# Optimization experiments

Hardware: AMD Instinct MI355X
Metric: run time of the kernel (lower is better)

Reference implementation:

```python
import jax, jax.numpy as jnp
import numpy as np

N_NODES = 50000
N_EDGES = 800000
F_IN = 128
HID = 128
OUT = 64


def setup_inputs() -> dict:
    key = jax.random.key(0)
    ks = jax.random.split(key, 10)
    def lin(k, fan_in, fan_out):
        s = 1.0 / np.sqrt(fan_in)
        kw, kb = jax.random.split(k)
        W = jax.random.uniform(kw, (fan_in, fan_out), jnp.float32, -s, s)
        b = jax.random.uniform(kb, (fan_out,), jnp.float32, -s, s)
        return W, b
    x = jax.random.normal(ks[0], (N_NODES, F_IN), jnp.float32)
    edge_index = jax.random.randint(ks[1], (2, N_EDGES), 0, N_NODES, dtype=jnp.int32)
    W1, b1 = lin(ks[2], F_IN, HID)   # GCNConv 1
    Wl, bl = lin(ks[3], HID, HID)    # linear_layers
    W2, b2 = lin(ks[4], HID, HID)    # GCNConv 2
    Wo, bo = lin(ks[5], HID, OUT)    # output_layers
    return {"x": x, "edge_index": edge_index, "W1": W1, "b1": b1,
            "Wl": Wl, "bl": bl, "W2": W2, "b2": b2, "Wo": Wo, "bo": bo}


def gcn_conv(x, src, dst, W, b, n_nodes):
    # PyG GCNConv: add self loops, symmetric norm D^-1/2 (A+I) D^-1/2 (x W) + b
    deg = jax.ops.segment_sum(jnp.ones_like(dst, dtype=x.dtype), dst, num_segments=n_nodes)
    dinv = jnp.where(deg > 0, jax.lax.rsqrt(jnp.maximum(deg, 1.0)), 0.0)
    norm = dinv[src] * dinv[dst]                     # [E+N]
    h = x @ W                                        # [N, H]
    msg = h[src] * norm[:, None]                     # [E+N, H]
    agg = jax.ops.segment_sum(msg, dst, num_segments=n_nodes)
    return agg + b


def reference(x, edge_index, W1, b1, Wl, bl, W2, b2, Wo, bo):
    n = x.shape[0]
    loops = jnp.arange(n, dtype=edge_index.dtype)
    src = jnp.concatenate([edge_index[0], loops])
    dst = jnp.concatenate([edge_index[1], loops])
    h = jnp.tanh(gcn_conv(x, src, dst, W1, b1, n))
    h = h @ Wl + bl
    h = jnp.tanh(gcn_conv(h, src, dst, W2, b2, n))
    h = h @ Wo + bo                                  # [N, OUT]
    # adaptive_max_pool1d over nodes -> [1, OUT]
    return jnp.max(h, axis=0, keepdims=True)
```

## Files before the change

### kernel.cpp

```cpp
#include <hip/hip_runtime.h>
#include <math.h>

#define F 128
#define OUTF 64
#define CAP 64

typedef __attribute__((ext_vector_type(8))) short short8;
typedef __attribute__((ext_vector_type(4))) float f32x4;

__device__ inline unsigned short bf16_rne(float f) {
    unsigned u = __float_as_uint(f);
    return (unsigned short)((u + 0x7FFFu + ((u >> 16) & 1u)) >> 16);
}
__device__ inline float bf16_to_f(unsigned short h) {
    return __uint_as_float((unsigned)h << 16);
}

__global__ __launch_bounds__(256)
void fill_kernel(const int* __restrict__ src, const int* __restrict__ dst,
                 int* __restrict__ cnt, int* __restrict__ slot, int E) {
    int e = blockIdx.x * 256 + threadIdx.x;
    if (e >= E) return;
    int s = src[e], d = dst[e];
    int pos = atomicAdd(&cnt[d], 1);
    if (pos < CAP) slot[(size_t)d * CAP + pos] = s;
}

__device__ inline void wsplit(float w, int k, int nn, short* Hh, short* Hl) {
    int c = k >> 5, hh = (k >> 3) & 3, kk = k & 7;
    int j = nn >> 4, col = nn & 15;
    int idx = (((j * 4 + c) * 4 + hh) * 16 + col) * 8 + kk;
    unsigned short hi = bf16_rne(w);
    Hh[idx] = (short)hi;
    Hl[idx] = (short)bf16_rne(w - bf16_to_f(hi));
}

__global__ __launch_bounds__(256)
void prep_kernel(const float* __restrict__ W1, const float* __restrict__ Wl,
                 const float* __restrict__ bl, const float* __restrict__ W2,
                 const float* __restrict__ Wo,
                 short* __restrict__ W1h, short* __restrict__ W1l,
                 short* __restrict__ Wfh, short* __restrict__ Wfl,
                 short* __restrict__ Woh, short* __restrict__ Wol,
                 float* __restrict__ bf, const int* __restrict__ cnt,
                 float* __restrict__ dinv, int n) {
    int bi = blockIdx.x, t = threadIdx.x;
    if (bi < 64) {
        int base = bi * 256 + t;
        int k = base >> 7, nn = base & 127;
        wsplit(W1[k * 128 + nn], k, nn, W1h, W1l);
    } else if (bi < 128) {
        int base = (bi - 64) * 256 + t;
        int k = base >> 7, nn = base & 127;
        float acc = 0.f;
        #pragma unroll 8
        for (int m = 0; m < 128; ++m)
            acc = fmaf(Wl[k * 128 + m], W2[m * 128 + nn], acc);
        wsplit(acc, k, nn, Wfh, Wfl);
    } else if (bi < 160) {
        int base = (bi - 128) * 256 + t;
        int k = base >> 6, nn = base & 63;
        wsplit(Wo[k * 64 + nn], k, nn, Woh, Wol);
    } else if (bi == 160) {
        if (t < 128) {
            float acc = 0.f;
            #pragma unroll 8
            for (int k = 0; k < 128; ++k)
                acc = fmaf(bl[k], W2[k * 128 + t], acc);
            bf[t] = acc;
        }
    } else {
        int i = (bi - 161) * 256 + t;
        if (i < n) dinv[i] = rsqrtf((float)cnt[i] + 1.0f);
    }
}

__global__ __launch_bounds__(256)
void gather_kernel(const float* __restrict__ H, const float* __restrict__ dinv,
                   const int* __restrict__ cnt, const int* __restrict__ slot,
                   const float* __restrict__ b, float* __restrict__ out, int n) {
    int wave = threadIdx.x >> 6;
    int lane = threadIdx.x & 63;
    int v = blockIdx.x * 4 + wave;
    if (v >= n) return;
    float dd = dinv[v];
    int deg = min(cnt[v], CAP);
    const int* sl = slot + (size_t)v * CAP;

    int s_l = 0; float nd_l = 0.f;
    if (lane < deg) { s_l = sl[lane]; nd_l = dinv[s_l] * dd; }

    float2 h0 = ((const float2*)(H + (size_t)v * F))[lane];
    float s2 = dd * dd;
    float ax = h0.x * s2, ay = h0.y * s2;

    int t = 0;
    for (; t + 4 <= deg; t += 4) {
        int s0 = __shfl(s_l, t),     s1 = __shfl(s_l, t + 1);
        int s2i = __shfl(s_l, t + 2), s3 = __shfl(s_l, t + 3);
        float n0 = __shfl(nd_l, t),     n1 = __shfl(nd_l, t + 1);
        float n2 = __shfl(nd_l, t + 2), n3 = __shfl(nd_l, t + 3);
        float2 u0 = ((const float2*)(H + (size_t)s0 * F))[lane];
        float2 u1 = ((const float2*)(H + (size_t)s1 * F))[lane];
        float2 u2 = ((const float2*)(H + (size_t)s2i * F))[lane];
        float2 u3 = ((const float2*)(H + (size_t)s3 * F))[lane];
        ax = fmaf(u0.x, n0, ax); ay = fmaf(u0.y, n0, ay);
        ax = fmaf(u1.x, n1, ax); ay = fmaf(u1.y, n1, ay);
        ax = fmaf(u2.x, n2, ax); ay = fmaf(u2.y, n2, ay);
        ax = fmaf(u3.x, n3, ax); ay = fmaf(u3.y, n3, ay);
    }
    for (; t < deg; ++t) {
        int s0 = __shfl(s_l, t);
        float n0 = __shfl(nd_l, t);
        float2 u0 = ((const float2*)(H + (size_t)s0 * F))[lane];
        ax = fmaf(u0.x, n0, ax); ay = fmaf(u0.y, n0, ay);
    }

    float2 bb = ((const float2*)b)[lane];
    float2 r;
    r.x = tanhf(ax + bb.x);
    r.y = tanhf(ay + bb.y);
    ((float2*)(out + (size_t)v * F))[lane] = r;
}

template<int COLS, bool BIAS, bool DOMAX>
__global__ __launch_bounds__(256)
void mgemm_kernel(const float* __restrict__ A, const short* __restrict__ Whi,
                  const short* __restrict__ Wlo, const float* __restrict__ bias,
                  float* __restrict__ C, float* __restrict__ part, int n) {
    constexpr int NT = COLS / 16;
    __shared__ float red[DOMAX ? 4 * COLS : 1];
    int t = threadIdx.x;
    int wave = t >> 6, l = t & 63;
    int fr = l & 15, fh = l >> 4;
    int m0 = blockIdx.x * 64 + wave * 16;
    int arow = min(m0 + fr, n - 1);
    const float* Ap = A + (size_t)arow * F + fh * 8;

    f32x4 acc[NT];
    #pragma unroll
    for (int j = 0; j < NT; ++j) acc[j] = (f32x4){0.f, 0.f, 0.f, 0.f};

    #pragma unroll
    for (int c = 0; c < 4; ++c) {
        float4 a0 = *(const float4*)(Ap + c * 32);
        float4 a1 = *(const float4*)(Ap + c * 32 + 4);
        short8 ahi, alo;
        {
            float v[8] = {a0.x, a0.y, a0.z, a0.w, a1.x, a1.y, a1.z, a1.w};
            #pragma unroll
            for (int i = 0; i < 8; ++i) {
                unsigned short hb = bf16_rne(v[i]);
                ahi[i] = (short)hb;
                alo[i] = (short)bf16_rne(v[i] - bf16_to_f(hb));
            }
        }
        #pragma unroll
        for (int j = 0; j < NT; ++j) {
            int bidx = (((j * 4 + c) * 4 + fh) * 16 + fr) * 8;
            short8 bhi = *(const short8*)(Whi + bidx);
            short8 blo = *(const short8*)(Wlo + bidx);
            acc[j] = __builtin_amdgcn_mfma_f32_16x16x32_bf16(ahi, bhi, acc[j], 0, 0, 0);
            acc[j] = __builtin_amdgcn_mfma_f32_16x16x32_bf16(alo, bhi, acc[j], 0, 0, 0);
            acc[j] = __builtin_amdgcn_mfma_f32_16x16x32_bf16(ahi, blo, acc[j], 0, 0, 0);
        }
    }

    float bv[NT];
    #pragma unroll
    for (int j = 0; j < NT; ++j) bv[j] = (BIAS || DOMAX) ? bias[j * 16 + fr] : 0.f;

    if (DOMAX) {
        #pragma unroll
        for (int j = 0; j < NT; ++j) {
            float mj = -INFINITY;
            #pragma unroll
            for (int reg = 0; reg < 4; ++reg) {
                int r = m0 + fh * 4 + reg;
                if (r < n) mj = fmaxf(mj, acc[j][reg] + bv[j]);
            }
            mj = fmaxf(mj, __shfl_xor(mj, 16));
            mj = fmaxf(mj, __shfl_xor(mj, 32));
            if (fh == 0) red[wave * COLS + j * 16 + fr] = mj;
        }
        __syncthreads();
        if (t < COLS) {
            float mm = fmaxf(fmaxf(red[t], red[COLS + t]),
                             fmaxf(red[2 * COLS + t], red[3 * COLS + t]));
            part[blockIdx.x * COLS + t] = mm;
        }
    } else {
        #pragma unroll
        for (int j = 0; j < NT; ++j) {
            int ccol = j * 16 + fr;
            #pragma unroll
            for (int reg = 0; reg < 4; ++reg) {
                int r = m0 + fh * 4 + reg;
                if (r < n) C[(size_t)r * COLS + ccol] = acc[j][reg] + bv[j];
            }
        }
    }
}

__global__ __launch_bounds__(256)
void rowmax_final(const float* __restrict__ part, float* __restrict__ out, int nb) {
    int c = threadIdx.x & 63;
    int g = threadIdx.x >> 6;
    float m = -INFINITY;
    for (int bidx = g; bidx < nb; bidx += 4)
        m = fmaxf(m, part[bidx * OUTF + c]);
    __shared__ float sm[256];
    sm[threadIdx.x] = m;
    __syncthreads();
    if (threadIdx.x < 64) {
        m = fmaxf(fmaxf(sm[threadIdx.x], sm[threadIdx.x + 64]),
                  fmaxf(sm[threadIdx.x + 128], sm[threadIdx.x + 192]));
        out[threadIdx.x] = m;
    }
}

extern "C" void kernel_launch(void* const* d_in, const int* in_sizes, int n_in,
                              void* d_out, int out_size, void* d_ws, size_t ws_size,
                              hipStream_t stream) {
    const float* x  = (const float*)d_in[0];
    const int*   ei = (const int*)d_in[1];
    const float* W1 = (const float*)d_in[2];
    const float* b1 = (const float*)d_in[3];
    const float* Wl = (const float*)d_in[4];
    const float* bl = (const float*)d_in[5];
    const float* W2 = (const float*)d_in[6];
    const float* b2 = (const float*)d_in[7];
    const float* Wo = (const float*)d_in[8];
    const float* bo = (const float*)d_in[9];

    int n = in_sizes[0] / F;
    int E = in_sizes[1] / 2;
    const int* src = ei;
    const int* dst = ei + E;

    auto align = [](size_t o) { return (o + 255) & ~(size_t)255; };
    char* ws = (char*)d_ws;
    size_t off = 0;
    size_t NB = (size_t)n * F * sizeof(float);
    float* bufA = (float*)(ws + off); off = align(off + NB);
    float* bufB = (float*)(ws + off); off = align(off + NB);
    float* dinv = (float*)(ws + off); off = align(off + (size_t)n * 4);
    int*   cnt  = (int*)(ws + off);   off = align(off + (size_t)n * 4);
    int*   slot = (int*)(ws + off);   off = align(off + (size_t)n * CAP * 4);
    float* bf   = (float*)(ws + off); off = align(off + 128 * 4);
    short* W1h  = (short*)(ws + off); off = align(off + 16384 * 2);
    short* W1l  = (short*)(ws + off); off = align(off + 16384 * 2);
    short* Wfh  = (short*)(ws + off); off = align(off + 16384 * 2);
    short* Wfl  = (short*)(ws + off); off = align(off + 16384 * 2);
    short* Woh  = (short*)(ws + off); off = align(off + 8192 * 2);
    short* Wol  = (short*)(ws + off); off = align(off + 8192 * 2);
    float* part = (float*)(ws + off); off = align(off + (size_t)800 * 64 * 4);

    int gE    = (E + 255) / 256;
    int gScan = (n + 255) / 256;
    int gGat  = (n + 3) / 4;
    int gM    = (n + 63) / 64;

    hipMemsetAsync(cnt, 0, (size_t)n * sizeof(int), stream);
    fill_kernel<<<gE, 256, 0, stream>>>(src, dst, cnt, slot, E);
    prep_kernel<<<161 + gScan, 256, 0, stream>>>(W1, Wl, bl, W2, Wo,
                                                 W1h, W1l, Wfh, Wfl, Woh, Wol,
                                                 bf, cnt, dinv, n);

    mgemm_kernel<128, false, false><<<gM, 256, 0, stream>>>(x, W1h, W1l, nullptr, bufA, nullptr, n);
    gather_kernel<<<gGat, 256, 0, stream>>>(bufA, dinv, cnt, slot, b1, bufB, n);

    mgemm_kernel<128, true, false><<<gM, 256, 0, stream>>>(bufB, Wfh, Wfl, bf, bufA, nullptr, n);
    gather_kernel<<<gGat, 256, 0, stream>>>(bufA, dinv, cnt, slot, b2, bufB, n);

    mgemm_kernel<64, true, true><<<gM, 256, 0, stream>>>(bufB, Woh, Wol, bo, nullptr, part, n);
    rowmax_final<<<1, 256, 0, stream>>>(part, (float*)d_out, gM);
}
```

Baseline: 330.7 us.

## Split gather across feature chunks with 16 edges per wave in parallel

The gather kernel is restructured so each block handles a 16-column feature chunk for 16 nodes. Within a wave, 16 edge groups of 4 lanes each load a float4 slice from different neighbors at once, and the partial sums are combined with xor-shuffle reductions. This is meant to raise memory-level parallelism on the irregular neighbor loads, which previously ran one edge at a time with float2 per lane. In exchange it adds shuffle reduction overhead, and the grid now touches each node's slot list and dinv from 8 separate blocks.

```diff
diff --git a/kernel.cpp b/kernel.cpp
--- a/kernel.cpp
+++ b/kernel.cpp
@@ -79,48 +79,55 @@
 void gather_kernel(const float* __restrict__ H, const float* __restrict__ dinv,
                    const int* __restrict__ cnt, const int* __restrict__ slot,
                    const float* __restrict__ b, float* __restrict__ out, int n) {
+    int chunk = blockIdx.x & 7;
+    int tile  = blockIdx.x >> 3;
     int wave = threadIdx.x >> 6;
     int lane = threadIdx.x & 63;
-    int v = blockIdx.x * 4 + wave;
-    if (v >= n) return;
-    float dd = dinv[v];
-    int deg = min(cnt[v], CAP);
-    const int* sl = slot + (size_t)v * CAP;
-
-    int s_l = 0; float nd_l = 0.f;
-    if (lane < deg) { s_l = sl[lane]; nd_l = dinv[s_l] * dd; }
-
-    float2 h0 = ((const float2*)(H + (size_t)v * F))[lane];
-    float s2 = dd * dd;
-    float ax = h0.x * s2, ay = h0.y * s2;
-
-    int t = 0;
-    for (; t + 4 <= deg; t += 4) {
-        int s0 = __shfl(s_l, t),     s1 = __shfl(s_l, t + 1);
-        int s2i = __shfl(s_l, t + 2), s3 = __shfl(s_l, t + 3);
-        float n0 = __shfl(nd_l, t),     n1 = __shfl(nd_l, t + 1);
-        float n2 = __shfl(nd_l, t + 2), n3 = __shfl(nd_l, t + 3);
-        float2 u0 = ((const float2*)(H + (size_t)s0 * F))[lane];
-        float2 u1 = ((const float2*)(H + (size_t)s1 * F))[lane];
-        float2 u2 = ((const float2*)(H + (size_t)s2i * F))[lane];
-        float2 u3 = ((const float2*)(H + (size_t)s3 * F))[lane];
-        ax = fmaf(u0.x, n0, ax); ay = fmaf(u0.y, n0, ay);
-        ax = fmaf(u1.x, n1, ax); ay = fmaf(u1.y, n1, ay);
-        ax = fmaf(u2.x, n2, ax); ay = fmaf(u2.y, n2, ay);
-        ax = fmaf(u3.x, n3, ax); ay = fmaf(u3.y, n3, ay);
-    }
-    for (; t < deg; ++t) {
-        int s0 = __shfl(s_l, t);
-        float n0 = __shfl(nd_l, t);
-        float2 u0 = ((const float2*)(H + (size_t)s0 * F))[lane];
-        ax = fmaf(u0.x, n0, ax); ay = fmaf(u0.y, n0, ay);
-    }
-
-    float2 bb = ((const float2*)b)[lane];
-    float2 r;
-    r.x = tanhf(ax + bb.x);
-    r.y = tanhf(ay + bb.y);
-    ((float2*)(out + (size_t)v * F))[lane] = r;
+    int eg = lane >> 2;
+    int cl = lane & 3;
+    int c0 = chunk * 16 + cl * 4;
+    float4 bb = *(const float4*)(b + c0);
+
+    #pragma unroll
+    for (int it = 0; it < 4; ++it) {
+        int v = tile * 16 + it * 4 + wave;
+        if (v >= n) return;
+        float dd = dinv[v];
+        int deg = min(cnt[v], CAP);
+        const int* sl = slot + (size_t)v * CAP;
+
+        int s_l = 0; float nd_l = 0.f;
+        if (lane < deg) { s_l = sl[lane]; nd_l = dinv[s_l] * dd; }
+
+        float ax = 0.f, ay = 0.f, az = 0.f, aw = 0.f;
+        for (int t0 = 0; t0 < deg; t0 += 16) {
+            int t = t0 + eg;
+            int s = __shfl(s_l, t);
+            float nn = __shfl(nd_l, t);
+            if (t < deg) {
+                float4 u = *(const float4*)(H + (size_t)s * F + c0);
+                ax = fmaf(u.x, nn, ax); ay = fmaf(u.y, nn, ay);
+                az = fmaf(u.z, nn, az); aw = fmaf(u.w, nn, aw);
+            }
+        }
+        #pragma unroll
+        for (int m = 4; m <= 32; m <<= 1) {
+            ax += __shfl_xor(ax, m); ay += __shfl_xor(ay, m);
+            az += __shfl_xor(az, m); aw += __shfl_xor(aw, m);
+        }
+        if (eg == 0) {
+            float4 h0 = *(const float4*)(H + (size_t)v * F + c0);
+            float s2 = dd * dd;
+            ax = fmaf(h0.x, s2, ax); ay = fmaf(h0.y, s2, ay);
+            az = fmaf(h0.z, s2, az); aw = fmaf(h0.w, s2, aw);
+            float4 r;
+            r.x = tanhf(ax + bb.x);
+            r.y = tanhf(ay + bb.y);
+            r.z = tanhf(az + bb.z);
+            r.w = tanhf(aw + bb.w);
+            *(float4*)(out + (size_t)v * F + c0) = r;
+        }
+    }
 }
 
 template<int COLS, bool BIAS, bool DOMAX>
@@ -258,7 +265,7 @@
 
     int gE    = (E + 255) / 256;
     int gScan = (n + 255) / 256;
-    int gGat  = (n + 3) / 4;
+    int gGat  = ((n + 15) / 16) * 8;
     int gM    = (n + 63) / 64;
 
     hipMemsetAsync(cnt, 0, (size_t)n * sizeof(int), stream);
```

New measurement: 466.4 us. +41.0%, slower.
